# Kernel optimization log

Measured on AMD Instinct MI355X. Metric: run time of the kernel, lower is better.

The kernel has to match this reference:

```python
import jax, jax.numpy as jnp
import numpy as np

B, S, D = 2, 2048, 2048
H, KVH = 16, 8
HD = D // H          # 128
REP = H // KVH       # 2
FF = 5504
EPS = 1e-5
THETA = 1e6


def rotate_half(x):
    h = x.shape[-1] // 2
    return jnp.concatenate([-x[..., h:], x[..., :h]], axis=-1)


def rms_norm(x, g):
    v = jnp.mean(x.astype(jnp.float32) ** 2, axis=-1, keepdims=True)
    return (x * jax.lax.rsqrt(v + EPS)).astype(x.dtype) * g


def setup_inputs() -> dict:
    key = jax.random.key(0)
    ks = jax.random.split(key, 10)
    # RoPE tables [S, HD]
    inv_freq = 1.0 / (THETA ** (np.arange(0, HD, 2, dtype=np.float32) / HD))
    t = np.arange(S, dtype=np.float32)
    freqs = np.outer(t, inv_freq)                      # [S, HD/2]
    emb = np.concatenate([freqs, freqs], axis=-1)      # [S, HD]
    sc = 0.02
    return {
        "x": jax.random.normal(ks[0], (B, S, D), jnp.float32),
        "cos": jnp.asarray(np.cos(emb)),
        "sin": jnp.asarray(np.sin(emb)),
        "wq": jax.random.normal(ks[1], (H * HD, D), jnp.float32) * sc,
        "wk": jax.random.normal(ks[2], (KVH * HD, D), jnp.float32) * sc,
        "wv": jax.random.normal(ks[3], (KVH * HD, D), jnp.float32) * sc,
        "wo": jax.random.normal(ks[4], (D, H * HD), jnp.float32) * sc,
        "w_gate": jax.random.normal(ks[5], (FF, D), jnp.float32) * sc,
        "w_up": jax.random.normal(ks[6], (FF, D), jnp.float32) * sc,
        "w_down": jax.random.normal(ks[7], (D, FF), jnp.float32) * sc,
        "g1": jnp.ones((D,), jnp.float32),
        "g2": jnp.ones((D,), jnp.float32),
    }


def reference(x, cos, sin, wq, wk, wv, wo, w_gate, w_up, w_down, g1, g2):
    # ---- attention sub-block ----
    h = rms_norm(x, g1)
    q = (h @ wq.T).reshape(B, S, H, HD)
    k = (h @ wk.T).reshape(B, S, KVH, HD)
    v = (h @ wv.T).reshape(B, S, KVH, HD)
    # RoPE: cos/sin [S,HD] -> broadcast over (B, S, heads, HD) via unsqueeze at head dim
    c = cos[:S][:, None, :]
    s = sin[:S][:, None, :]
    q = q * c + rotate_half(q) * s
    k = k * c + rotate_half(k) * s
    # GQA repeat_kv (repeat_interleave on head dim), then bshd -> bhsd
    k = jnp.repeat(k, REP, axis=2).transpose(0, 2, 1, 3)
    v = jnp.repeat(v, REP, axis=2).transpose(0, 2, 1, 3)
    q = q.transpose(0, 2, 1, 3)
    scores = jnp.einsum("bhqd,bhkd->bhqk", q, k) / jnp.sqrt(jnp.float32(HD))
    causal = jnp.triu(jnp.full((S, S), -jnp.inf, jnp.float32), k=1)
    scores = scores + causal[None, None]
    attn = jax.nn.softmax(scores.astype(jnp.float32), axis=-1).astype(scores.dtype)
    out = jnp.einsum("bhqk,bhkd->bhqd", attn, v)
    out = out.transpose(0, 2, 1, 3).reshape(B, S, H * HD)
    x = x + out @ wo.T
    # ---- SwiGLU MLP sub-block ----
    h2 = rms_norm(x, g2)
    mlp = (jax.nn.silu(h2 @ w_gate.T) * (h2 @ w_up.T)) @ w_down.T
    return x + mlp
```

## Files before the change

kernel.cpp:

```cpp
#include <hip/hip_runtime.h>

#define DM 2048
#define SEQ 2048
#define HD 128
#define FF_ 5504
#define QK_SCALE_L2E 0.12751744f

typedef __bf16 bf16x8 __attribute__((ext_vector_type(8)));
typedef float f32x4 __attribute__((ext_vector_type(4)));
typedef float f32x16 __attribute__((ext_vector_type(16)));
typedef unsigned short u16x8 __attribute__((ext_vector_type(8)));
typedef unsigned int u32x4 __attribute__((ext_vector_type(4)));

typedef __attribute__((address_space(1))) void* gas1;
typedef __attribute__((address_space(3))) void* las3;
#define GLDS16(g, s) __builtin_amdgcn_global_load_lds((gas1)(g), (las3)(s), 16, 0, 0)

static __device__ __forceinline__ float bf2f(unsigned short u) {
  union { unsigned int i; float f; } c; c.i = ((unsigned int)u) << 16; return c.f;
}
static __device__ __forceinline__ unsigned short f2bf(float f) {
  __bf16 b = (__bf16)f;
  return __builtin_bit_cast(unsigned short, b);
}
static __device__ __forceinline__ unsigned int pk2(float a, float b) {
  return (unsigned int)f2bf(a) | ((unsigned int)f2bf(b) << 16);
}
static __device__ __forceinline__ float fexp2(float x) { return exp2f(x); }

__global__ __launch_bounds__(256) void k_convW(const float* __restrict__ wq,
                                               const float* __restrict__ wk,
                                               const float* __restrict__ wv,
                                               const float* __restrict__ wo,
                                               unsigned short* __restrict__ wqkv,
                                               unsigned short* __restrict__ wo_bf) {
  int b = blockIdx.x;
  const float* src;
  unsigned short* dst;
  if (b < 2048)      { src = wq + (size_t)b * DM;            dst = wqkv + (size_t)b * DM; }
  else if (b < 3072) { src = wk + (size_t)(b - 2048) * DM;   dst = wqkv + 4194304 + (size_t)(b - 2048) * DM; }
  else if (b < 4096) { src = wv + (size_t)(b - 3072) * DM;   dst = wqkv + 6291456 + (size_t)(b - 3072) * DM; }
  else               { src = wo + (size_t)(b - 4096) * DM;   dst = wo_bf + (size_t)(b - 4096) * DM; }
  int i = threadIdx.x * 8;
  float4 a = *(const float4*)&src[i];
  float4 c = *(const float4*)&src[i + 4];
  u16x8 o;
  o[0] = f2bf(a.x); o[1] = f2bf(a.y); o[2] = f2bf(a.z); o[3] = f2bf(a.w);
  o[4] = f2bf(c.x); o[5] = f2bf(c.y); o[6] = f2bf(c.z); o[7] = f2bf(c.w);
  *(u16x8*)&dst[i] = o;
}

__global__ __launch_bounds__(256) void k_conv(const float* __restrict__ src,
                                              unsigned short* __restrict__ dst) {
  size_t i = (size_t)(blockIdx.x * 256 + threadIdx.x) * 8;
  float4 a = *(const float4*)&src[i];
  float4 b = *(const float4*)&src[i + 4];
  u16x8 o;
  o[0] = f2bf(a.x); o[1] = f2bf(a.y); o[2] = f2bf(a.z); o[3] = f2bf(a.w);
  o[4] = f2bf(b.x); o[5] = f2bf(b.y); o[6] = f2bf(b.z); o[7] = f2bf(b.w);
  *(u16x8*)&dst[i] = o;
}

__global__ __launch_bounds__(256) void k_conv_gu(const float* __restrict__ g,
                                                 const float* __restrict__ u,
                                                 unsigned short* __restrict__ dst) {
  int i = blockIdx.x * 256 + threadIdx.x;
  int row = i >> 8;
  int c8 = (i & 255) * 8;
  int t = row >> 8, r = row & 255;
  const float* src = (r < 128) ? (g + (size_t)(t * 128 + r) * DM + c8)
                               : (u + (size_t)(t * 128 + (r - 128)) * DM + c8);
  float4 a = *(const float4*)src;
  float4 b = *(const float4*)(src + 4);
  u16x8 o;
  o[0] = f2bf(a.x); o[1] = f2bf(a.y); o[2] = f2bf(a.z); o[3] = f2bf(a.w);
  o[4] = f2bf(b.x); o[5] = f2bf(b.y); o[6] = f2bf(b.z); o[7] = f2bf(b.w);
  *(u16x8*)&dst[(size_t)row * DM + c8] = o;
}

__global__ __launch_bounds__(256) void k_rmsnorm(const float* __restrict__ x,
                                                 const float* __restrict__ g,
                                                 unsigned short* __restrict__ out) {
  int row = blockIdx.x, tid = threadIdx.x;
  const float* xr = x + (size_t)row * DM;
  float4 a = *(const float4*)&xr[tid * 8];
  float4 b = *(const float4*)&xr[tid * 8 + 4];
  float ss = a.x * a.x + a.y * a.y + a.z * a.z + a.w * a.w +
             b.x * b.x + b.y * b.y + b.z * b.z + b.w * b.w;
#pragma unroll
  for (int off = 32; off > 0; off >>= 1) ss += __shfl_xor(ss, off, 64);
  __shared__ float red[4];
  if ((tid & 63) == 0) red[tid >> 6] = ss;
  __syncthreads();
  float rs = rsqrtf((red[0] + red[1] + red[2] + red[3]) * (1.0f / DM) + 1e-5f);
  float4 ga = *(const float4*)&g[tid * 8];
  float4 gb = *(const float4*)&g[tid * 8 + 4];
  u16x8 o;
  o[0] = f2bf(a.x * rs * ga.x); o[1] = f2bf(a.y * rs * ga.y);
  o[2] = f2bf(a.z * rs * ga.z); o[3] = f2bf(a.w * rs * ga.w);
  o[4] = f2bf(b.x * rs * gb.x); o[5] = f2bf(b.y * rs * gb.y);
  o[6] = f2bf(b.z * rs * gb.z); o[7] = f2bf(b.w * rs * gb.w);
  *(u16x8*)&out[(size_t)row * DM + tid * 8] = o;
}

template <int EPI>
__global__ __launch_bounds__(512, 1) void k_gemm8p(
    const unsigned short* __restrict__ A, const unsigned short* __restrict__ Bt,
    unsigned short* __restrict__ outB, float* __restrict__ outF,
    const float* __restrict__ res, int N, int K,
    const float* __restrict__ cosT, const float* __restrict__ sinT) {
  __shared__ __attribute__((aligned(16))) unsigned char smem[2][65536];
  const int tid = threadIdx.x, w = tid >> 6, l = tid & 63;
  const int wr = w >> 2, wc = w & 3, lr = l & 15, lg = l >> 4;
  const int bswz = blockIdx.x;
  const int mt = bswz & 15, nt = bswz >> 4;
  const int m0 = mt * 256, n0 = nt * 256;
  const int nkt = K >> 6;

  const int rA0 = tid >> 3;
  const int rB0 = ((tid >> 8) << 6) + ((tid >> 3) & 31);
  const int sc = ((tid & 7) ^ ((tid >> 3) & 7)) * 8;
  const unsigned short* Abase = A + (size_t)(m0 + rA0) * K + sc;
  const unsigned short* Bbase = Bt + (size_t)(n0 + rB0) * K + sc;

  auto stA = [&](int kt, int h) {
    unsigned char* dst = smem[kt & 1] + h * 16384;
    const unsigned short* s = Abase + (size_t)(h * 64) * K + kt * 64;
    GLDS16(s, dst + tid * 16);
    GLDS16(s + (size_t)128 * K, dst + (512 + tid) * 16);
  };
  auto stB = [&](int kt, int h) {
    unsigned char* dst = smem[kt & 1] + 32768 + h * 16384;
    const unsigned short* s = Bbase + (size_t)(h * 32) * K + kt * 64;
    GLDS16(s, dst + tid * 16);
    GLDS16(s + (size_t)128 * K, dst + (512 + tid) * 16);
  };

  const int aRow = (wr * 64 + lr) * 128;
  const int bRow = (wc * 32 + lr) * 128;
  const int axr = lr & 7;
#define RDA(BUF, M, KK)                                                        \
  (*(const bf16x8*)((BUF) + ((M) >> 2) * 16384 + aRow + ((M) & 3) * 2048 +     \
                    ((((KK) * 4 + lg) ^ axr) << 4)))
#define RDB(BUF, NN, KK)                                                       \
  (*(const bf16x8*)((BUF) + 32768 + ((NN) >> 1) * 16384 + bRow +               \
                    ((NN) & 1) * 2048 + ((((KK) * 4 + lg) ^ axr) << 4)))

  f32x4 acc[8][4] = {};
  bf16x8 aq[4][2], bq0[2][2], bq1[2][2];

  stA(0, 0); stB(0, 0); stB(0, 1); stA(0, 1);
  stA(1, 0); stB(1, 0); stB(1, 1);
  asm volatile("s_waitcnt vmcnt(6)" ::: "memory");
  __builtin_amdgcn_s_barrier();

#define MMQ(MB, NB, BQ)                                                        \
  _Pragma("unroll") for (int m = 0; m < 4; m++)                                \
    _Pragma("unroll") for (int n = 0; n < 2; n++)                              \
      _Pragma("unroll") for (int kk = 0; kk < 2; kk++)                         \
          acc[(MB) + m][(NB) + n] = __builtin_amdgcn_mfma_f32_16x16x32_bf16(   \
              aq[m][kk], BQ[n][kk], acc[(MB) + m][(NB) + n], 0, 0, 0);

#define KTQ(KT, ST1, ST2, W2V, HASW2, W4V, HASW4)                              \
  {                                                                            \
    const unsigned char* buf = smem[(KT) & 1];                                 \
           \
    _Pragma("unroll") for (int m = 0; m < 4; m++)                              \
      _Pragma("unroll") for (int kk = 0; kk < 2; kk++)                         \
          aq[m][kk] = RDA(buf, m, kk);                                         \
    _Pragma("unroll") for (int n = 0; n < 2; n++)                              \
      _Pragma("unroll") for (int kk = 0; kk < 2; kk++)                         \
          bq0[n][kk] = RDB(buf, n, kk);                                        \
    _Pragma("unroll") for (int n = 0; n < 2; n++)                              \
      _Pragma("unroll") for (int kk = 0; kk < 2; kk++)                         \
          bq1[n][kk] = RDB(buf, n + 2, kk);                                    \
    if (ST1) stA((KT) + 1, 1);                                                 \
    asm volatile("s_waitcnt lgkmcnt(4)" ::: "memory");                         \
    __builtin_amdgcn_sched_barrier(0);                                         \
    __builtin_amdgcn_s_setprio(1);                                             \
    MMQ(0, 0, bq0)                                                             \
    __builtin_amdgcn_s_setprio(0);                                             \
    __builtin_amdgcn_s_barrier();                                              \
                     \
    if (ST2) stA((KT) + 2, 0);                                                 \
    asm volatile("s_waitcnt lgkmcnt(0)" ::: "memory");                         \
    __builtin_amdgcn_sched_barrier(0);                                         \
    __builtin_amdgcn_s_setprio(1);                                             \
    MMQ(0, 2, bq1)                                                             \
    __builtin_amdgcn_s_setprio(0);                                             \
    if (HASW2) asm volatile("s_waitcnt vmcnt(%0)" ::"i"(W2V) : "memory");      \
    __builtin_amdgcn_s_barrier();                                              \
                            \
    _Pragma("unroll") for (int m = 0; m < 4; m++)                              \
      _Pragma("unroll") for (int kk = 0; kk < 2; kk++)                         \
          aq[m][kk] = RDA(buf, m + 4, kk);                                     \
    if (ST2) stB((KT) + 2, 0);                                                 \
    asm volatile("s_waitcnt lgkmcnt(0)" ::: "memory");                         \
    __builtin_amdgcn_sched_barrier(0);                                         \
    __builtin_amdgcn_s_setprio(1);                                             \
    MMQ(4, 2, bq1)                                                             \
    __builtin_amdgcn_s_setprio(0);                                             \
    __builtin_amdgcn_s_barrier();                                              \
              \
    if (ST2) stB((KT) + 2, 1);                                                 \
    __builtin_amdgcn_s_setprio(1);                                             \
    MMQ(4, 0, bq0)                                                             \
    __builtin_amdgcn_s_setprio(0);                                             \
    if (HASW4) asm volatile("s_waitcnt vmcnt(%0)" ::"i"(W4V) : "memory");      \
    __builtin_amdgcn_s_barrier();                                              \
  }

  for (int kt = 0; kt < nkt - 2; kt++) KTQ(kt, 1, 1, 6, 1, 6, 1);
  KTQ(nkt - 2, 1, 0, 4, 1, 0, 1);
  KTQ(nkt - 1, 0, 0, 0, 0, 0, 0);
#undef KTQ
#undef MMQ
#undef RDA
#undef RDB

  const int rbase = wr * 128 + lg * 4;
  const int cbase = wc * 64 + lr;
  if constexpr (EPI == 0) {
#pragma unroll
    for (int m = 0; m < 8; m++)
#pragma unroll
      for (int n = 0; n < 4; n++)
#pragma unroll
        for (int j = 0; j < 4; j++)
          outB[(size_t)(m0 + rbase + m * 16 + j) * N + n0 + cbase + n * 16] =
              f2bf(acc[m][n][j]);
  } else if constexpr (EPI == 1) {
#pragma unroll
    for (int m = 0; m < 8; m++)
#pragma unroll
      for (int n = 0; n < 4; n++)
#pragma unroll
        for (int j = 0; j < 4; j++) {
          size_t o = (size_t)(m0 + rbase + m * 16 + j) * N + n0 + cbase + n * 16;
          outF[o] = res[o] + acc[m][n][j];
        }
  } else if constexpr (EPI == 2) {
    float* gl = (float*)smem;
    const int ab = n0 >> 1;
    __syncthreads();
#pragma unroll
    for (int half = 0; half < 2; half++) {
      if (wr == half && wc < 2) {
#pragma unroll
        for (int m = 0; m < 8; m++)
#pragma unroll
          for (int n = 0; n < 4; n++)
#pragma unroll
            for (int j = 0; j < 4; j++)
              gl[(m * 16 + lg * 4 + j) * 128 + wc * 64 + n * 16 + lr] = acc[m][n][j];
      }
      __syncthreads();
      if (wr == half && wc >= 2) {
#pragma unroll
        for (int m = 0; m < 8; m++)
#pragma unroll
          for (int n = 0; n < 4; n++)
#pragma unroll
            for (int j = 0; j < 4; j++) {
              int rl = m * 16 + lg * 4 + j;
              int cl = (wc - 2) * 64 + n * 16 + lr;
              float g = gl[rl * 128 + cl];
              float s = g / (1.0f + __expf(-g));
              outB[(size_t)(m0 + half * 128 + rl) * FF_ + ab + cl] = f2bf(s * acc[m][n][j]);
            }
      }
      __syncthreads();
    }
  } else {
    if (nt >= 12) {
#pragma unroll
      for (int m = 0; m < 8; m++)
#pragma unroll
        for (int n = 0; n < 4; n++)
#pragma unroll
          for (int j = 0; j < 4; j++)
            outB[(size_t)(m0 + rbase + m * 16 + j) * N + n0 + cbase + n * 16] =
                f2bf(acc[m][n][j]);
    } else {
      float* gl = (float*)smem;
      const float qs = (nt < 8) ? QK_SCALE_L2E : 1.0f;
      __syncthreads();
      for (int m = 0; m < 8; m++) {
#pragma unroll
        for (int n = 0; n < 4; n++)
#pragma unroll
          for (int j = 0; j < 4; j++)
            gl[wr * 4096 + (lg * 4 + j) * 256 + wc * 64 + n * 16 + lr] = acc[m][n][j];
        __syncthreads();
#pragma unroll
        for (int n = 0; n < 4; n++)
#pragma unroll
          for (int j = 0; j < 4; j++) {
            int c = wc * 64 + n * 16 + lr;
            int d = c & 127;
            int row = m0 + wr * 128 + m * 16 + lg * 4 + j;
            int s = row & (SEQ - 1);
            float own = acc[m][n][j];
            float prt = gl[wr * 4096 + (lg * 4 + j) * 256 + (c ^ 64)];
            float cv = cosT[s * HD + d], sv = sinT[s * HD + d];
            float rot = own * cv + ((d & 64) ? prt : -prt) * sv;
            outB[(size_t)row * N + n0 + c] = f2bf(rot * qs);
          }
        __syncthreads();
      }
    }
  }
}

template <int BN, int EPI>
__global__ __launch_bounds__(512, 2) void k_gemm8(
    const unsigned short* __restrict__ A, const unsigned short* __restrict__ Bt,
    unsigned short* __restrict__ outB, float* __restrict__ outF,
    const float* __restrict__ res, int N, int K) {
  constexpr int NF = BN / 64;
  constexpr int BSTMT = BN / 128;
  constexpr int ABY = 256 * 64;
  constexpr int BBY = BN * 64;
  constexpr int BUF = ABY + BBY;
  constexpr int VPK = 2 + BSTMT;
  __shared__ __attribute__((aligned(16))) unsigned char smem[4 * BUF];

  const int tid = threadIdx.x, w = tid >> 6, l = tid & 63;
  const int wr = w >> 2, wc = w & 3, lr = l & 15, lg = l >> 4;
  const int bswz = blockIdx.x;
  const int mt = bswz & 15, nt = bswz >> 4;
  const int m0 = mt * 256, n0 = nt * BN;
  const int nk = K >> 5;

  const int srow = w * 16 + (l >> 2);
  const int sg8 = ((l & 3) ^ ((l >> 3) & 3)) * 8;
  const unsigned short* Asrc = A + (size_t)(m0 + srow) * K + sg8;
  const unsigned short* Bsrc = Bt + (size_t)(n0 + srow) * K + sg8;
  const int aoff = (wr * 128 + lr) * 64 + ((lg ^ ((lr >> 1) & 3)) << 4);
  const int boff = (wc * (BN / 4) + lr) * 64 + ((lg ^ ((lr >> 1) & 3)) << 4);

  auto stageA = [&](int kt) {
    unsigned char* bb = smem + (kt & 3) * BUF;
#pragma unroll
    for (int i = 0; i < 2; i++)
      GLDS16(Asrc + (size_t)i * 128 * K + kt * 32, bb + (i * 512 + w * 64) * 16);
  };
  auto stageB = [&](int kt) {
    unsigned char* bb = smem + (kt & 3) * BUF + ABY;
#pragma unroll
    for (int i = 0; i < BSTMT; i++)
      GLDS16(Bsrc + (size_t)i * 128 * K + kt * 32, bb + (i * 512 + w * 64) * 16);
  };

  f32x4 acc[8][NF] = {};

  for (int kt = 0; kt < 3; kt++) { stageA(kt); stageB(kt); }
  asm volatile("s_waitcnt vmcnt(%0)" ::"i"(2 * VPK) : "memory");
  __builtin_amdgcn_s_barrier();
  for (int kt = 0; kt < nk; kt++) {
    unsigned char* ba = smem + (kt & 3) * BUF;
    unsigned char* bb = ba + ABY;
    const bool st = (kt + 3) < nk;
    bf16x8 am[8], bnf[NF];
#pragma unroll
    for (int m = 0; m < 8; m++) am[m] = *(const bf16x8*)(ba + aoff + m * 1024);
#pragma unroll
    for (int n = 0; n < NF; n++) bnf[n] = *(const bf16x8*)(bb + boff + n * 1024);
    if (st) { stageA(kt + 3); stageB(kt + 3); }
    __builtin_amdgcn_s_barrier();
    __builtin_amdgcn_s_setprio(1);
#pragma unroll
    for (int m = 0; m < 8; m++)
#pragma unroll
      for (int n = 0; n < NF; n++)
        acc[m][n] = __builtin_amdgcn_mfma_f32_16x16x32_bf16(am[m], bnf[n], acc[m][n], 0, 0, 0);
    __builtin_amdgcn_s_setprio(0);
    if (kt <= nk - 4)      asm volatile("s_waitcnt vmcnt(%0)" ::"i"(2 * VPK) : "memory");
    else if (kt == nk - 3) asm volatile("s_waitcnt vmcnt(%0)" ::"i"(VPK) : "memory");
    else if (kt == nk - 2) asm volatile("s_waitcnt vmcnt(0)" ::: "memory");
    __builtin_amdgcn_s_barrier();
  }

  const int rbase = wr * 128 + lg * 4;
  const int cbase = wc * (BN / 4) + lr;
  if constexpr (EPI == 0) {
#pragma unroll
    for (int m = 0; m < 8; m++)
#pragma unroll
      for (int n = 0; n < NF; n++)
#pragma unroll
        for (int j = 0; j < 4; j++)
          outB[(size_t)(m0 + rbase + m * 16 + j) * N + n0 + cbase + n * 16] =
              f2bf(acc[m][n][j]);
  } else {
#pragma unroll
    for (int m = 0; m < 8; m++)
#pragma unroll
      for (int n = 0; n < NF; n++)
#pragma unroll
        for (int j = 0; j < 4; j++) {
          size_t o = (size_t)(m0 + rbase + m * 16 + j) * N + n0 + cbase + n * 16;
          outF[o] = res[o] + acc[m][n][j];
        }
  }
}

__global__ __launch_bounds__(256) void k_attn2(const unsigned short* __restrict__ qkv,
                                               unsigned short* __restrict__ out) {
  __shared__ __attribute__((aligned(16))) unsigned short lK[2][64 * 128];
  __shared__ __attribute__((aligned(16))) unsigned short lV[2][128 * 64];
  const float NEG = -3.0e38f;
  int bx = blockIdx.x;
  int qtile = 15 - (bx >> 5);
  int hb = bx & 31;
  int h = hb & 15, b = hb >> 4;
  int q0 = qtile * 128;
  int tid = threadIdx.x, w = tid >> 6, l = tid & 63;
  int l31 = l & 31, half2 = l >> 5;
  const unsigned short* base = qkv + (size_t)b * SEQ * 4096;
  const unsigned short* Kp = base + 2048 + (h >> 1) * HD;
  const unsigned short* Vp = base + 3072 + (h >> 1) * HD;
  const int qw = q0 + w * 32;

  bf16x8 qf[8];
  {
    const unsigned short* qrow = base + (size_t)(qw + l31) * 4096 + h * HD + half2 * 8;
#pragma unroll
    for (int d = 0; d < 8; d++) qf[d] = *(const bf16x8*)(qrow + d * 16);
  }

  f32x16 oacc[4] = {};
  float mrow = NEG, lsum = 0.0f;

  const int vp = tid & 31, vdc = tid >> 5;
  u16x8 va0, va1, vb0, vb1;

  auto stageK = [&](int t) {
    unsigned char* dst = (unsigned char*)lK[t & 1];
#pragma unroll
    for (int i = 0; i < 4; i++) {
      int c = i * 256 + tid;
      int row = c >> 4;
      int g = (c & 15) ^ (row & 7);
      GLDS16(Kp + (size_t)(t * 64 + row) * 4096 + g * 8, dst + (i * 256 + w * 64) * 16);
    }
  };
  auto loadV = [&](int t) {
    const unsigned short* vr = Vp + (size_t)(t * 64 + vp * 2) * 4096 + vdc * 16;
    va0 = *(const u16x8*)(vr);
    va1 = *(const u16x8*)(vr + 8);
    vb0 = *(const u16x8*)(vr + 4096);
    vb1 = *(const u16x8*)(vr + 4096 + 8);
  };

  const int nt = (q0 >> 6) + 2;
  stageK(0);
  loadV(0);

  for (int t = 0; t < nt; t++) {
    __syncthreads();
    {
      unsigned char* lv = (unsigned char*)lV[t & 1];
#pragma unroll
      for (int j = 0; j < 16; j++) {
        int dd = vdc * 16 + j;
        unsigned short lo = (j < 8) ? va0[j] : va1[j - 8];
        unsigned short hi = (j < 8) ? vb0[j] : vb1[j - 8];
        unsigned int pkv = (unsigned int)lo | ((unsigned int)hi << 16);
        *(unsigned int*)(lv + dd * 128 + (((vp >> 2) ^ (dd & 7)) * 16) + (vp & 3) * 4) = pkv;
      }
    }
    __syncthreads();
    if (t + 1 < nt) { stageK(t + 1); loadV(t + 1); }
    const int kv0 = t * 64;
    if (kv0 <= qw + 31) {
      f32x16 sc[2] = {};
      const unsigned char* lk = (const unsigned char*)lK[t & 1];
#pragma unroll
      for (int hh = 0; hh < 2; hh++) {
        int kk = hh * 32 + l31;
        const unsigned char* krow = lk + kk * 256;
#pragma unroll
        for (int d = 0; d < 8; d++) {
          bf16x8 kf = *(const bf16x8*)(krow + (((d * 2 + half2) ^ (kk & 7)) * 16));
          sc[hh] = __builtin_amdgcn_mfma_f32_32x32x16_bf16(kf, qf[d], sc[hh], 0, 0, 0);
        }
      }
      const int qa = qw + l31;
      if (kv0 + 63 > qw) {
#pragma unroll
        for (int hh = 0; hh < 2; hh++)
#pragma unroll
          for (int r = 0; r < 16; r++) {
            int kva = kv0 + hh * 32 + (r & 3) + 8 * (r >> 2) + 4 * half2;
            if (kva > qa) sc[hh][r] = NEG;
          }
      }
      float mx = sc[0][0];
#pragma unroll
      for (int r = 1; r < 16; r++) mx = fmaxf(mx, sc[0][r]);
#pragma unroll
      for (int r = 0; r < 16; r++) mx = fmaxf(mx, sc[1][r]);
      mx = fmaxf(mx, __shfl_xor(mx, 32));
      bool ok = (mx <= mrow + 11.0f);
      if (__ballot(ok) != ~0ull) {
        float mnew = fmaxf(mrow, mx);
        float fct = fexp2(mrow - mnew);
        mrow = mnew;
        lsum *= fct;
#pragma unroll
        for (int r = 0; r < 16; r++) {
          int rr = (r & 3) + 8 * (r >> 2) + 4 * half2;
          float fr = __shfl(fct, rr);
#pragma unroll
          for (int d = 0; d < 4; d++) oacc[d][r] *= fr;
        }
      }
      float ps = 0.0f;
#pragma unroll
      for (int hh = 0; hh < 2; hh++)
#pragma unroll
        for (int r = 0; r < 16; r++) {
          float e = fexp2(sc[hh][r] - mrow);
          sc[hh][r] = e;
          ps += e;
        }
      ps += __shfl_xor(ps, 32);
      lsum += ps;
      const unsigned char* lv = (const unsigned char*)lV[t & 1];
#pragma unroll
      for (int s = 0; s < 4; s++) {
        const int hh = s >> 1;
        const int r0 = (s & 1) * 8;
        unsigned int lo0, lo1, hi0, hi1;
        if (hh == 0) {
          lo0 = pk2(sc[0][r0 + 0], sc[0][r0 + 1]); lo1 = pk2(sc[0][r0 + 2], sc[0][r0 + 3]);
          hi0 = pk2(sc[0][r0 + 4], sc[0][r0 + 5]); hi1 = pk2(sc[0][r0 + 6], sc[0][r0 + 7]);
        } else {
          lo0 = pk2(sc[1][r0 + 0], sc[1][r0 + 1]); lo1 = pk2(sc[1][r0 + 2], sc[1][r0 + 3]);
          hi0 = pk2(sc[1][r0 + 4], sc[1][r0 + 5]); hi1 = pk2(sc[1][r0 + 6], sc[1][r0 + 7]);
        }
        unsigned int s0 = half2 ? lo0 : hi0, s1 = half2 ? lo1 : hi1;
        unsigned int rc0 = (unsigned int)__shfl_xor((int)s0, 32);
        unsigned int rc1 = (unsigned int)__shfl_xor((int)s1, 32);
        u32x4 fr;
        fr[0] = half2 ? rc0 : lo0; fr[1] = half2 ? rc1 : lo1;
        fr[2] = half2 ? hi0 : rc0; fr[3] = half2 ? hi1 : rc1;
        bf16x8 pa = __builtin_bit_cast(bf16x8, fr);
#pragma unroll
        for (int d = 0; d < 4; d++) {
          int dd = d * 32 + l31;
          bf16x8 vf = *(const bf16x8*)(lv + dd * 128 + (((s * 2 + half2) ^ (dd & 7)) * 16));
          oacc[d] = __builtin_amdgcn_mfma_f32_32x32x16_bf16(pa, vf, oacc[d], 0, 0, 0);
        }
      }
    }
  }
  float inv = 1.0f / lsum;
#pragma unroll
  for (int r = 0; r < 16; r++) {
    int rr = (r & 3) + 8 * (r >> 2) + 4 * half2;
    float ir = __shfl(inv, rr);
    size_t ob = ((size_t)(b * SEQ + qw + rr)) * 2048 + h * HD;
#pragma unroll
    for (int d = 0; d < 4; d++)
      out[ob + d * 32 + l31] = f2bf(oacc[d][r] * ir);
  }
}

extern "C" void kernel_launch(void* const* d_in, const int* in_sizes, int n_in,
                              void* d_out, int out_size, void* d_ws, size_t ws_size,
                              hipStream_t stream) {
  const float* x = (const float*)d_in[0];
  const float* cosT = (const float*)d_in[1];
  const float* sinT = (const float*)d_in[2];
  const float* wq = (const float*)d_in[3];
  const float* wk = (const float*)d_in[4];
  const float* wv = (const float*)d_in[5];
  const float* wo = (const float*)d_in[6];
  const float* wg = (const float*)d_in[7];
  const float* wu = (const float*)d_in[8];
  const float* wd = (const float*)d_in[9];
  const float* g1 = (const float*)d_in[10];
  const float* g2 = (const float*)d_in[11];
  float* out = (float*)d_out;
  char* ws = (char*)d_ws;

  unsigned short* wqkv = (unsigned short*)(ws + 0);
  unsigned short* hbuf = (unsigned short*)(ws + 16777216);
  unsigned short* qkv = (unsigned short*)(ws + 33554432);
  unsigned short* attn_o = (unsigned short*)(ws + 67108864);
  unsigned short* wo_bf = (unsigned short*)(ws + 83886080);
  unsigned short* wgu = (unsigned short*)(ws + 33554432);
  unsigned short* act = (unsigned short*)(ws + 92274688);
  unsigned short* wdown = (unsigned short*)(ws + 0);

  k_convW<<<6144, 256, 0, stream>>>(wq, wk, wv, wo, wqkv, wo_bf);
  k_rmsnorm<<<4096, 256, 0, stream>>>(x, g1, hbuf);
  k_gemm8p<3><<<256, 512, 0, stream>>>(hbuf, wqkv, qkv, nullptr, nullptr,
                                       4096, 2048, cosT, sinT);
  k_attn2<<<512, 256, 0, stream>>>(qkv, attn_o);
  k_gemm8<128, 1><<<256, 512, 0, stream>>>(attn_o, wo_bf, nullptr, out, x,
                                           2048, 2048);
  k_rmsnorm<<<4096, 256, 0, stream>>>(out, g2, hbuf);
  k_conv_gu<<<11008, 256, 0, stream>>>(wg, wu, wgu);
  k_gemm8p<2><<<688, 512, 0, stream>>>(hbuf, wgu, act, nullptr, nullptr,
                                       11008, 2048, nullptr, nullptr);
  k_conv<<<5504, 256, 0, stream>>>(wd, wdown);
  k_gemm8<128, 1><<<256, 512, 0, stream>>>(act, wdown, nullptr, out, out,
                                           2048, 5504);
}
```

Before: 583.1 us.

## Route BN=128 output-projection and down GEMMs through 8-phase pipelined kernel

Extends the ping-pong, phase-split GEMM kernel with a BN=128 variant that uses a 64-wide K step, double buffering and split A halves. It replaces the older 4-stage k_gemm8 for the Wo and down projections. The goal is better overlap of LDS reads, global-to-LDS loads and MFMA work through setprio and barrier-interleaved phases. In exchange, occupancy drops from 2 blocks per CU to 1 (launch_bounds 512,1), and the pipeline has only two stages. K=5504 is divisible by 64 (86 steps), so the K loop covers it exactly.

Measured after the change: 565.6 us. -3.0%, faster.

```diff
diff --git a/kernel.cpp b/kernel.cpp
--- a/kernel.cpp
+++ b/kernel.cpp
@@ -103,22 +103,24 @@
   *(u16x8*)&out[(size_t)row * DM + tid * 8] = o;
 }
 
-template <int EPI>
+template <int BN, int EPI>
 __global__ __launch_bounds__(512, 1) void k_gemm8p(
     const unsigned short* __restrict__ A, const unsigned short* __restrict__ Bt,
     unsigned short* __restrict__ outB, float* __restrict__ outF,
     const float* __restrict__ res, int N, int K,
     const float* __restrict__ cosT, const float* __restrict__ sinT) {
-  __shared__ __attribute__((aligned(16))) unsigned char smem[2][65536];
+  constexpr int NF = BN / 64;
+  constexpr int BUFSZ = (BN == 256) ? 65536 : 49152;
+  __shared__ __attribute__((aligned(16))) unsigned char smem[2][BUFSZ];
   const int tid = threadIdx.x, w = tid >> 6, l = tid & 63;
   const int wr = w >> 2, wc = w & 3, lr = l & 15, lg = l >> 4;
   const int bswz = blockIdx.x;
   const int mt = bswz & 15, nt = bswz >> 4;
-  const int m0 = mt * 256, n0 = nt * 256;
+  const int m0 = mt * 256, n0 = nt * BN;
   const int nkt = K >> 6;
 
   const int rA0 = tid >> 3;
-  const int rB0 = ((tid >> 8) << 6) + ((tid >> 3) & 31);
+  const int rB0 = (BN == 256) ? (((tid >> 8) << 6) + ((tid >> 3) & 31)) : (tid >> 3);
   const int sc = ((tid & 7) ^ ((tid >> 3) & 7)) * 8;
   const unsigned short* Abase = A + (size_t)(m0 + rA0) * K + sc;
   const unsigned short* Bbase = Bt + (size_t)(n0 + rB0) * K + sc;
@@ -135,6 +137,12 @@
     GLDS16(s, dst + tid * 16);
     GLDS16(s + (size_t)128 * K, dst + (512 + tid) * 16);
   };
+  auto stB2 = [&](int kt) {
+    unsigned char* dst = smem[kt & 1] + 32768;
+    const unsigned short* s = Bbase + kt * 64;
+    GLDS16(s, dst + tid * 16);
+    GLDS16(s + (size_t)64 * K, dst + (512 + tid) * 16);
+  };
 
   const int aRow = (wr * 64 + lr) * 128;
   const int bRow = (wc * 32 + lr) * 128;
@@ -146,13 +154,14 @@
   (*(const bf16x8*)((BUF) + 32768 + ((NN) >> 1) * 16384 + bRow +               \
                     ((NN) & 1) * 2048 + ((((KK) * 4 + lg) ^ axr) << 4)))
 
-  f32x4 acc[8][4] = {};
-  bf16x8 aq[4][2], bq0[2][2], bq1[2][2];
-
-  stA(0, 0); stB(0, 0); stB(0, 1); stA(0, 1);
-  stA(1, 0); stB(1, 0); stB(1, 1);
-  asm volatile("s_waitcnt vmcnt(6)" ::: "memory");
-  __builtin_amdgcn_s_barrier();
+  f32x4 acc[8][NF] = {};
+
+  if constexpr (BN == 256) {
+    bf16x8 aq[4][2], bq0[2][2], bq1[2][2];
+    stA(0, 0); stB(0, 0); stB(0, 1); stA(0, 1);
+    stA(1, 0); stB(1, 0); stB(1, 1);
+    asm volatile("s_waitcnt vmcnt(6)" ::: "memory");
+    __builtin_amdgcn_s_barrier();
 
 #define MMQ(MB, NB, BQ)                                                        \
   _Pragma("unroll") for (int m = 0; m < 4; m++)                                \
@@ -164,7 +173,6 @@
 #define KTQ(KT, ST1, ST2, W2V, HASW2, W4V, HASW4)                              \
   {                                                                            \
     const unsigned char* buf = smem[(KT) & 1];                                 \
-           \
     _Pragma("unroll") for (int m = 0; m < 4; m++)                              \
       _Pragma("unroll") for (int kk = 0; kk < 2; kk++)                         \
           aq[m][kk] = RDA(buf, m, kk);                                         \
@@ -181,7 +189,6 @@
     MMQ(0, 0, bq0)                                                             \
     __builtin_amdgcn_s_setprio(0);                                             \
     __builtin_amdgcn_s_barrier();                                              \
-                     \
     if (ST2) stA((KT) + 2, 0);                                                 \
     asm volatile("s_waitcnt lgkmcnt(0)" ::: "memory");                         \
     __builtin_amdgcn_sched_barrier(0);                                         \
@@ -190,7 +197,6 @@
     __builtin_amdgcn_s_setprio(0);                                             \
     if (HASW2) asm volatile("s_waitcnt vmcnt(%0)" ::"i"(W2V) : "memory");      \
     __builtin_amdgcn_s_barrier();                                              \
-                            \
     _Pragma("unroll") for (int m = 0; m < 4; m++)                              \
       _Pragma("unroll") for (int kk = 0; kk < 2; kk++)                         \
           aq[m][kk] = RDA(buf, m + 4, kk);                                     \
@@ -201,7 +207,6 @@
     MMQ(4, 2, bq1)                                                             \
     __builtin_amdgcn_s_setprio(0);                                             \
     __builtin_amdgcn_s_barrier();                                              \
-              \
     if (ST2) stB((KT) + 2, 1);                                                 \
     __builtin_amdgcn_s_setprio(1);                                             \
     MMQ(4, 0, bq0)                                                             \
@@ -210,21 +215,71 @@
     __builtin_amdgcn_s_barrier();                                              \
   }
 
-  for (int kt = 0; kt < nkt - 2; kt++) KTQ(kt, 1, 1, 6, 1, 6, 1);
-  KTQ(nkt - 2, 1, 0, 4, 1, 0, 1);
-  KTQ(nkt - 1, 0, 0, 0, 0, 0, 0);
+    for (int kt = 0; kt < nkt - 2; kt++) KTQ(kt, 1, 1, 6, 1, 6, 1);
+    KTQ(nkt - 2, 1, 0, 4, 1, 0, 1);
+    KTQ(nkt - 1, 0, 0, 0, 0, 0, 0);
 #undef KTQ
 #undef MMQ
+  } else {
+    bf16x8 alo[4][2], ahi[4][2], bq[2][2];
+    stA(0, 0); stB2(0); stA(0, 1); stA(1, 0); stB2(1);
+    asm volatile("s_waitcnt vmcnt(4)" ::: "memory");
+    __builtin_amdgcn_s_barrier();
+
+#define MM2(MB, AQ)                                                            \
+  _Pragma("unroll") for (int m = 0; m < 4; m++)                                \
+    _Pragma("unroll") for (int n = 0; n < 2; n++)                              \
+      _Pragma("unroll") for (int kk = 0; kk < 2; kk++)                         \
+          acc[(MB) + m][n] = __builtin_amdgcn_mfma_f32_16x16x32_bf16(          \
+              AQ[m][kk], bq[n][kk], acc[(MB) + m][n], 0, 0, 0);
+
+#define KT2(KT, ST1, ST2, HASW, WV)                                            \
+  {                                                                            \
+    const unsigned char* buf = smem[(KT) & 1];                                 \
+                     \
+    _Pragma("unroll") for (int m = 0; m < 4; m++)                              \
+      _Pragma("unroll") for (int kk = 0; kk < 2; kk++)                         \
+          alo[m][kk] = RDA(buf, m, kk);                                        \
+    _Pragma("unroll") for (int n = 0; n < 2; n++)                              \
+      _Pragma("unroll") for (int kk = 0; kk < 2; kk++)                         \
+          bq[n][kk] = RDB(buf, n, kk);                                         \
+    _Pragma("unroll") for (int m = 0; m < 4; m++)                              \
+      _Pragma("unroll") for (int kk = 0; kk < 2; kk++)                         \
+          ahi[m][kk] = RDA(buf, m + 4, kk);                                    \
+    if (ST1) stA((KT) + 1, 1);                                                 \
+    asm volatile("s_waitcnt lgkmcnt(8)" ::: "memory");                         \
+    __builtin_amdgcn_sched_barrier(0);                                         \
+    __builtin_amdgcn_s_setprio(1);                                             \
+    MM2(0, alo)                                                                \
+    __builtin_amdgcn_s_setprio(0);                                             \
+    __builtin_amdgcn_s_barrier();                                              \
+          \
+    if (ST2) { stA((KT) + 2, 0); stB2((KT) + 2); }                             \
+    asm volatile("s_waitcnt lgkmcnt(0)" ::: "memory");                         \
+    __builtin_amdgcn_sched_barrier(0);                                         \
+    __builtin_amdgcn_s_setprio(1);                                             \
+    MM2(4, ahi)                                                                \
+    __builtin_amdgcn_s_setprio(0);                                             \
+    if (HASW) asm volatile("s_waitcnt vmcnt(%0)" ::"i"(WV) : "memory");        \
+    __builtin_amdgcn_s_barrier();                                              \
+  }
+
+    for (int kt = 0; kt < nkt - 2; kt++) KT2(kt, 1, 1, 1, 4);
+    KT2(nkt - 2, 1, 0, 1, 0);
+    KT2(nkt - 1, 0, 0, 0, 0);
+#undef KT2
+#undef MM2
+  }
 #undef RDA
 #undef RDB
 
   const int rbase = wr * 128 + lg * 4;
-  const int cbase = wc * 64 + lr;
+  const int cbase = wc * (BN / 4) + lr;
   if constexpr (EPI == 0) {
 #pragma unroll
     for (int m = 0; m < 8; m++)
 #pragma unroll
-      for (int n = 0; n < 4; n++)
+      for (int n = 0; n < NF; n++)
 #pragma unroll
         for (int j = 0; j < 4; j++)
           outB[(size_t)(m0 + rbase + m * 16 + j) * N + n0 + cbase + n * 16] =
@@ -233,7 +288,7 @@
 #pragma unroll
     for (int m = 0; m < 8; m++)
 #pragma unroll
-      for (int n = 0; n < 4; n++)
+      for (int n = 0; n < NF; n++)
 #pragma unroll
         for (int j = 0; j < 4; j++) {
           size_t o = (size_t)(m0 + rbase + m * 16 + j) * N + n0 + cbase + n * 16;
@@ -249,7 +304,7 @@
 #pragma unroll
         for (int m = 0; m < 8; m++)
 #pragma unroll
-          for (int n = 0; n < 4; n++)
+          for (int n = 0; n < NF; n++)
 #pragma unroll
             for (int j = 0; j < 4; j++)
               gl[(m * 16 + lg * 4 + j) * 128 + wc * 64 + n * 16 + lr] = acc[m][n][j];
@@ -259,7 +314,7 @@
 #pragma unroll
         for (int m = 0; m < 8; m++)
 #pragma unroll
-          for (int n = 0; n < 4; n++)
+          for (int n = 0; n < NF; n++)
 #pragma unroll
             for (int j = 0; j < 4; j++) {
               int rl = m * 16 + lg * 4 + j;
@@ -276,7 +331,7 @@
 #pragma unroll
       for (int m = 0; m < 8; m++)
 #pragma unroll
-        for (int n = 0; n < 4; n++)
+        for (int n = 0; n < NF; n++)
 #pragma unroll
           for (int j = 0; j < 4; j++)
             outB[(size_t)(m0 + rbase + m * 16 + j) * N + n0 + cbase + n * 16] =
@@ -287,13 +342,13 @@
       __syncthreads();
       for (int m = 0; m < 8; m++) {
 #pragma unroll
-        for (int n = 0; n < 4; n++)
+        for (int n = 0; n < NF; n++)
 #pragma unroll
           for (int j = 0; j < 4; j++)
             gl[wr * 4096 + (lg * 4 + j) * 256 + wc * 64 + n * 16 + lr] = acc[m][n][j];
         __syncthreads();
 #pragma unroll
-        for (int n = 0; n < 4; n++)
+        for (int n = 0; n < NF; n++)
 #pragma unroll
           for (int j = 0; j < 4; j++) {
             int c = wc * 64 + n * 16 + lr;
@@ -309,99 +364,6 @@
         __syncthreads();
       }
     }
-  }
-}
-
-template <int BN, int EPI>
-__global__ __launch_bounds__(512, 2) void k_gemm8(
-    const unsigned short* __restrict__ A, const unsigned short* __restrict__ Bt,
-    unsigned short* __restrict__ outB, float* __restrict__ outF,
-    const float* __restrict__ res, int N, int K) {
-  constexpr int NF = BN / 64;
-  constexpr int BSTMT = BN / 128;
-  constexpr int ABY = 256 * 64;
-  constexpr int BBY = BN * 64;
-  constexpr int BUF = ABY + BBY;
-  constexpr int VPK = 2 + BSTMT;
-  __shared__ __attribute__((aligned(16))) unsigned char smem[4 * BUF];
-
-  const int tid = threadIdx.x, w = tid >> 6, l = tid & 63;
-  const int wr = w >> 2, wc = w & 3, lr = l & 15, lg = l >> 4;
-  const int bswz = blockIdx.x;
-  const int mt = bswz & 15, nt = bswz >> 4;
-  const int m0 = mt * 256, n0 = nt * BN;
-  const int nk = K >> 5;
-
-  const int srow = w * 16 + (l >> 2);
-  const int sg8 = ((l & 3) ^ ((l >> 3) & 3)) * 8;
-  const unsigned short* Asrc = A + (size_t)(m0 + srow) * K + sg8;
-  const unsigned short* Bsrc = Bt + (size_t)(n0 + srow) * K + sg8;
-  const int aoff = (wr * 128 + lr) * 64 + ((lg ^ ((lr >> 1) & 3)) << 4);
-  const int boff = (wc * (BN / 4) + lr) * 64 + ((lg ^ ((lr >> 1) & 3)) << 4);
-
-  auto stageA = [&](int kt) {
-    unsigned char* bb = smem + (kt & 3) * BUF;
-#pragma unroll
-    for (int i = 0; i < 2; i++)
-      GLDS16(Asrc + (size_t)i * 128 * K + kt * 32, bb + (i * 512 + w * 64) * 16);
-  };
-  auto stageB = [&](int kt) {
-    unsigned char* bb = smem + (kt & 3) * BUF + ABY;
-#pragma unroll
-    for (int i = 0; i < BSTMT; i++)
-      GLDS16(Bsrc + (size_t)i * 128 * K + kt * 32, bb + (i * 512 + w * 64) * 16);
-  };
-
-  f32x4 acc[8][NF] = {};
-
-  for (int kt = 0; kt < 3; kt++) { stageA(kt); stageB(kt); }
-  asm volatile("s_waitcnt vmcnt(%0)" ::"i"(2 * VPK) : "memory");
-  __builtin_amdgcn_s_barrier();
-  for (int kt = 0; kt < nk; kt++) {
-    unsigned char* ba = smem + (kt & 3) * BUF;
-    unsigned char* bb = ba + ABY;
-    const bool st = (kt + 3) < nk;
-    bf16x8 am[8], bnf[NF];
-#pragma unroll
-    for (int m = 0; m < 8; m++) am[m] = *(const bf16x8*)(ba + aoff + m * 1024);
-#pragma unroll
-    for (int n = 0; n < NF; n++) bnf[n] = *(const bf16x8*)(bb + boff + n * 1024);
-    if (st) { stageA(kt + 3); stageB(kt + 3); }
-    __builtin_amdgcn_s_barrier();
-    __builtin_amdgcn_s_setprio(1);
-#pragma unroll
-    for (int m = 0; m < 8; m++)
-#pragma unroll
-      for (int n = 0; n < NF; n++)
-        acc[m][n] = __builtin_amdgcn_mfma_f32_16x16x32_bf16(am[m], bnf[n], acc[m][n], 0, 0, 0);
-    __builtin_amdgcn_s_setprio(0);
-    if (kt <= nk - 4)      asm volatile("s_waitcnt vmcnt(%0)" ::"i"(2 * VPK) : "memory");
-    else if (kt == nk - 3) asm volatile("s_waitcnt vmcnt(%0)" ::"i"(VPK) : "memory");
-    else if (kt == nk - 2) asm volatile("s_waitcnt vmcnt(0)" ::: "memory");
-    __builtin_amdgcn_s_barrier();
-  }
-
-  const int rbase = wr * 128 + lg * 4;
-  const int cbase = wc * (BN / 4) + lr;
-  if constexpr (EPI == 0) {
-#pragma unroll
-    for (int m = 0; m < 8; m++)
-#pragma unroll
-      for (int n = 0; n < NF; n++)
-#pragma unroll
-        for (int j = 0; j < 4; j++)
-          outB[(size_t)(m0 + rbase + m * 16 + j) * N + n0 + cbase + n * 16] =
-              f2bf(acc[m][n][j]);
-  } else {
-#pragma unroll
-    for (int m = 0; m < 8; m++)
-#pragma unroll
-      for (int n = 0; n < NF; n++)
-#pragma unroll
-        for (int j = 0; j < 4; j++) {
-          size_t o = (size_t)(m0 + rbase + m * 16 + j) * N + n0 + cbase + n * 16;
-          outF[o] = res[o] + acc[m][n][j];
-        }
   }
 }
 
@@ -597,16 +559,16 @@
 
   k_convW<<<6144, 256, 0, stream>>>(wq, wk, wv, wo, wqkv, wo_bf);
   k_rmsnorm<<<4096, 256, 0, stream>>>(x, g1, hbuf);
-  k_gemm8p<3><<<256, 512, 0, stream>>>(hbuf, wqkv, qkv, nullptr, nullptr,
-                                       4096, 2048, cosT, sinT);
+  k_gemm8p<256, 3><<<256, 512, 0, stream>>>(hbuf, wqkv, qkv, nullptr, nullptr,
+                                            4096, 2048, cosT, sinT);
   k_attn2<<<512, 256, 0, stream>>>(qkv, attn_o);
-  k_gemm8<128, 1><<<256, 512, 0, stream>>>(attn_o, wo_bf, nullptr, out, x,
-                                           2048, 2048);
+  k_gemm8p<128, 1><<<256, 512, 0, stream>>>(attn_o, wo_bf, nullptr, out, x,
+                                            2048, 2048, nullptr, nullptr);
   k_rmsnorm<<<4096, 256, 0, stream>>>(out, g2, hbuf);
   k_conv_gu<<<11008, 256, 0, stream>>>(wg, wu, wgu);
-  k_gemm8p<2><<<688, 512, 0, stream>>>(hbuf, wgu, act, nullptr, nullptr,
-                                       11008, 2048, nullptr, nullptr);
+  k_gemm8p<256, 2><<<688, 512, 0, stream>>>(hbuf, wgu, act, nullptr, nullptr,
+                                            11008, 2048, nullptr, nullptr);
   k_conv<<<5504, 256, 0, stream>>>(wd, wdown);
-  k_gemm8<128, 1><<<256, 512, 0, stream>>>(act, wdown, nullptr, out, out,
-                                           2048, 5504);
-}
+  k_gemm8p<128, 1><<<256, 512, 0, stream>>>(act, wdown, nullptr, out, out,
+                                            2048, 5504, nullptr, nullptr);
+}
```
